# Kernel tuning notes

Measured on AMD Instinct MI355X. Metric: run time of the kernel, lower is better.

## Reference

```python
import jax, jax.numpy as jnp
import numpy as np

NACT = 4  # len(activation_list): [linear, cos, sin, tan]


def setup_inputs() -> dict:
    key = jax.random.key(0)
    kx, kw = jax.random.split(key)
    size_in, size_out, batch = 256, 1024, 131072
    x = jax.random.normal(kx, (batch, size_in), dtype=jnp.float32)
    # kaiming_uniform_ with a=sqrt(5): bound = sqrt(6/((1+a^2)*fan_in)) = 1/sqrt(fan_in)
    bound = 1.0 / np.sqrt(size_in)
    weight = jax.random.uniform(kw, (size_out, size_in), dtype=jnp.float32,
                                minval=-bound, maxval=bound)
    return {"x": x, "weight": weight}


def reference(x, weight):
    # linear_combo = x @ W^T : [B, size_out]
    y = jnp.matmul(x, weight.T)
    B, O = y.shape
    # Column j gets activation_list[j % NACT]; reshape so last axis = j % NACT.
    y3 = y.reshape(B, O // NACT, NACT)
    out = jnp.stack(
        [y3[..., 0],            # linear
         jnp.cos(y3[..., 1]),   # cos
         jnp.sin(y3[..., 2]),   # sin
         jnp.tan(y3[..., 3])],  # tan
        axis=-1,
    )
    return out.reshape(B, O)
```

## Files before the change

### kernel.cpp

```cpp
#include <hip/hip_runtime.h>
#include <math.h>

#define BATCH 131072
#define KDIM  256
#define ODIM  1024

#define BM 128
#define BN 128
#define BK 32
#define PAD 4

#define NROWT (BATCH / BM)
#define NCOLT (ODIM / BN)
#define NXCD  8

typedef float vfloat4 __attribute__((ext_vector_type(4)));

__global__ __launch_bounds__(256) void gemm_act(
    const float* __restrict__ x,
    const float* __restrict__ w,
    float* __restrict__ out)
{
    __shared__ float As[BK][BM + PAD];
    __shared__ float Bs[BK][BN + PAD];

    const int bid     = blockIdx.x;
    const int xcd     = bid & (NXCD - 1);
    const int j       = bid >> 3;
    const int rowtile = xcd * (NROWT / NXCD) + (j >> 3);
    const int coltile = j & (NCOLT - 1);
    const int row0    = rowtile * BM;
    const int col0    = coltile * BN;

    const int tid = threadIdx.x;
    const int ty  = (tid >> 4) << 2;
    const int tx  = (tid & 15) << 2;

    float acc[8][8] = {};

    for (int k0 = 0; k0 < KDIM; k0 += BK) {
        #pragma unroll
        for (int l = 0; l < 4; ++l) {
            const int f  = tid + l * 256;
            const int r  = f >> 3;
            const int k4 = (f & 7) << 2;
            float4 va = *(const float4*)(x + (size_t)(row0 + r) * KDIM + k0 + k4);
            float4 vb = *(const float4*)(w + (size_t)(col0 + r) * KDIM + k0 + k4);
            As[k4 + 0][r] = va.x; As[k4 + 1][r] = va.y;
            As[k4 + 2][r] = va.z; As[k4 + 3][r] = va.w;
            Bs[k4 + 0][r] = vb.x; Bs[k4 + 1][r] = vb.y;
            Bs[k4 + 2][r] = vb.z; Bs[k4 + 3][r] = vb.w;
        }
        __syncthreads();

        #pragma unroll 8
        for (int k = 0; k < BK; ++k) {
            float4 a0 = *(const float4*)&As[k][ty];
            float4 a1 = *(const float4*)&As[k][64 + ty];
            float4 b0 = *(const float4*)&Bs[k][tx];
            float4 b1 = *(const float4*)&Bs[k][64 + tx];
            const float ar[8] = {a0.x, a0.y, a0.z, a0.w, a1.x, a1.y, a1.z, a1.w};
            const float br[8] = {b0.x, b0.y, b0.z, b0.w, b1.x, b1.y, b1.z, b1.w};
            #pragma unroll
            for (int i = 0; i < 8; ++i)
                #pragma unroll
                for (int jj = 0; jj < 8; ++jj)
                    acc[i][jj] = fmaf(ar[i], br[jj], acc[i][jj]);
        }
        __syncthreads();
    }

    #pragma unroll
    for (int i = 0; i < 8; ++i) {
        const int row = row0 + (i < 4 ? ty + i : 64 + ty + (i - 4));
        #pragma unroll
        for (int jh = 0; jh < 2; ++jh) {
            const int colb = col0 + jh * 64 + tx;
            const float y0 = acc[i][jh * 4 + 0];
            const float y1 = acc[i][jh * 4 + 1];
            const float y2 = acc[i][jh * 4 + 2];
            const float y3 = acc[i][jh * 4 + 3];

            vfloat4 o;
            o.x = y0;
            o.y = __cosf(y1);
            o.z = __sinf(y2);
            o.w = tanf(y3);

            const float m    = rintf(y3 * 0.31830988618379067f);
            const float r2   = fmaf(-m, 3.14159265358979323f, y3);
            const float dist = fabsf(fabsf(r2) - 1.57079632679489662f);
            if (dist < 1e-2f) {
                o.w = (float)tan((double)y3);
            }

            __builtin_nontemporal_store(o, (vfloat4*)(out + (size_t)row * ODIM + colb));
        }
    }
}

extern "C" void kernel_launch(void* const* d_in, const int* in_sizes, int n_in,
                              void* d_out, int out_size, void* d_ws, size_t ws_size,
                              hipStream_t stream)
{
    const float* x = (const float*)d_in[0];
    const float* w = (const float*)d_in[1];
    float* out = (float*)d_out;

    dim3 grid(NROWT * NCOLT);
    gemm_act<<<grid, 256, 0, stream>>>(x, w, out);
}
```

Before: 1.246 ms.

## Load GEMM tiles directly into LDS with XOR-swizzled k-major layout

Global-to-shared tile loads now use global_load_lds (direct DMA into LDS), removing the register staging and scalar transposed LDS stores. Tiles are kept row-major along K, with an XOR swizzle on 16-byte chunks so the inner product can read vec4 slices along K without bank conflicts. The inner loop is rewritten to load A and B as k-vectors and do 4 K-steps per group. This trades the transposed, padded layout for more LDS read instructions per FMA and depends on the direct-to-LDS builtin lowering correctly on this target.

```diff
diff --git a/kernel.cpp b/kernel.cpp
--- a/kernel.cpp
+++ b/kernel.cpp
@@ -1,5 +1,6 @@
 #include <hip/hip_runtime.h>
 #include <math.h>
+#include <stdint.h>
 
 #define BATCH 131072
 #define KDIM  256
@@ -8,66 +9,96 @@
 #define BM 128
 #define BN 128
 #define BK 32
-#define PAD 4
-
+#define NTILE (KDIM / BK)
 #define NROWT (BATCH / BM)
 #define NCOLT (ODIM / BN)
 #define NXCD  8
 
-typedef float vfloat4 __attribute__((ext_vector_type(4)));
+typedef float vf4 __attribute__((ext_vector_type(4)));
+typedef const __attribute__((address_space(1))) uint32_t* gas1_t;
+typedef __attribute__((address_space(3)))       uint32_t* las3_t;
 
 __global__ __launch_bounds__(256) void gemm_act(
     const float* __restrict__ x,
     const float* __restrict__ w,
     float* __restrict__ out)
 {
-    __shared__ float As[BK][BM + PAD];
-    __shared__ float Bs[BK][BN + PAD];
+    __shared__ float As[BM * BK];
+    __shared__ float Bs[BN * BK];
 
     const int bid     = blockIdx.x;
     const int xcd     = bid & (NXCD - 1);
-    const int j       = bid >> 3;
-    const int rowtile = xcd * (NROWT / NXCD) + (j >> 3);
-    const int coltile = j & (NCOLT - 1);
+    const int jb      = bid >> 3;
+    const int rowtile = xcd * (NROWT / NXCD) + (jb >> 3);
+    const int coltile = jb & (NCOLT - 1);
     const int row0    = rowtile * BM;
     const int col0    = coltile * BN;
 
-    const int tid = threadIdx.x;
-    const int ty  = (tid >> 4) << 2;
-    const int tx  = (tid & 15) << 2;
+    const int tid  = threadIdx.x;
+    const int wave = tid >> 6;
+    const int lane = tid & 63;
+    const int lr   = lane >> 3;
+    const int ls   = lane & 7;
+
+    const float* srcA[4];
+    const float* srcB[4];
+    #pragma unroll
+    for (int m = 0; m < 4; ++m) {
+        const int r = wave * 32 + m * 8 + lr;
+        const int c = (ls ^ ((r >> 2) & 7)) << 2;
+        srcA[m] = x + (size_t)(row0 + r) * KDIM + c;
+        srcB[m] = w + (size_t)(col0 + r) * KDIM + c;
+    }
+
+    const int ty = (tid >> 4) << 2;
+    const int tx = (tid & 15) << 2;
+    const int tA = (tid >> 4) & 7;
+    const int tB = tid & 7;
 
     float acc[8][8] = {};
 
-    for (int k0 = 0; k0 < KDIM; k0 += BK) {
+    #pragma unroll
+    for (int t = 0; t < NTILE; ++t) {
+        __syncthreads();
+
         #pragma unroll
-        for (int l = 0; l < 4; ++l) {
-            const int f  = tid + l * 256;
-            const int r  = f >> 3;
-            const int k4 = (f & 7) << 2;
-            float4 va = *(const float4*)(x + (size_t)(row0 + r) * KDIM + k0 + k4);
-            float4 vb = *(const float4*)(w + (size_t)(col0 + r) * KDIM + k0 + k4);
-            As[k4 + 0][r] = va.x; As[k4 + 1][r] = va.y;
-            As[k4 + 2][r] = va.z; As[k4 + 3][r] = va.w;
-            Bs[k4 + 0][r] = vb.x; Bs[k4 + 1][r] = vb.y;
-            Bs[k4 + 2][r] = vb.z; Bs[k4 + 3][r] = vb.w;
+        for (int m = 0; m < 4; ++m) {
+            __builtin_amdgcn_global_load_lds(
+                (gas1_t)(const void*)(srcA[m] + t * BK),
+                (las3_t)(void*)&As[(wave * 32 + m * 8) * BK], 16, 0, 0);
+            __builtin_amdgcn_global_load_lds(
+                (gas1_t)(const void*)(srcB[m] + t * BK),
+                (las3_t)(void*)&Bs[(wave * 32 + m * 8) * BK], 16, 0, 0);
         }
         __syncthreads();
 
-        #pragma unroll 8
-        for (int k = 0; k < BK; ++k) {
-            float4 a0 = *(const float4*)&As[k][ty];
-            float4 a1 = *(const float4*)&As[k][64 + ty];
-            float4 b0 = *(const float4*)&Bs[k][tx];
-            float4 b1 = *(const float4*)&Bs[k][64 + tx];
-            const float ar[8] = {a0.x, a0.y, a0.z, a0.w, a1.x, a1.y, a1.z, a1.w};
-            const float br[8] = {b0.x, b0.y, b0.z, b0.w, b1.x, b1.y, b1.z, b1.w};
+        #pragma unroll
+        for (int g = 0; g < 8; ++g) {
+            const int cA = (g ^ tA) << 2;
+            const int cB = (g ^ tB) << 2;
+
+            vf4 A[8];
             #pragma unroll
-            for (int i = 0; i < 8; ++i)
+            for (int i = 0; i < 4; ++i) {
+                A[i]     = *(const vf4*)&As[(ty + i) * BK + cA];
+                A[4 + i] = *(const vf4*)&As[(64 + ty + i) * BK + cA];
+            }
+            #pragma unroll
+            for (int jh = 0; jh < 2; ++jh) {
+                vf4 B[4];
                 #pragma unroll
-                for (int jj = 0; jj < 8; ++jj)
-                    acc[i][jj] = fmaf(ar[i], br[jj], acc[i][jj]);
+                for (int j = 0; j < 4; ++j)
+                    B[j] = *(const vf4*)&Bs[(jh * 64 + tx + j) * BK + cB];
+                #pragma unroll
+                for (int kk = 0; kk < 4; ++kk)
+                    #pragma unroll
+                    for (int i = 0; i < 8; ++i)
+                        #pragma unroll
+                        for (int j = 0; j < 4; ++j)
+                            acc[i][jh * 4 + j] =
+                                fmaf(A[i][kk], B[j][kk], acc[i][jh * 4 + j]);
+            }
         }
-        __syncthreads();
     }
 
     #pragma unroll
@@ -81,20 +112,20 @@
             const float y2 = acc[i][jh * 4 + 2];
             const float y3 = acc[i][jh * 4 + 3];
 
-            vfloat4 o;
+            vf4 o;
             o.x = y0;
             o.y = __cosf(y1);
             o.z = __sinf(y2);
             o.w = tanf(y3);
 
-            const float m    = rintf(y3 * 0.31830988618379067f);
-            const float r2   = fmaf(-m, 3.14159265358979323f, y3);
+            const float m_   = rintf(y3 * 0.31830988618379067f);
+            const float r2   = fmaf(-m_, 3.14159265358979323f, y3);
             const float dist = fabsf(fabsf(r2) - 1.57079632679489662f);
             if (dist < 1e-2f) {
                 o.w = (float)tan((double)y3);
             }
 
-            __builtin_nontemporal_store(o, (vfloat4*)(out + (size_t)row * ODIM + colb));
+            __builtin_nontemporal_store(o, (vf4*)(out + (size_t)row * ODIM + colb));
         }
     }
 }
```

After: 3.478 ms. 2.79x slower.
